# Performance work log

Measured on AMD Instinct MI355X. Metric: run time of the kernel, lower is better.

Reference implementation:

```python
import jax, jax.numpy as jnp
import numpy as np

CH = 128          # channels
R1 = 8            # ch_reduction1 -> theta/phi dim = 16
R2 = 2            # ch_reduction2 -> g dim = 64
D = 2             # downsampling (maxpool kernel/stride on w,h)


def _conv1x1x1(x, w, b):
    # x: (b, cin, n, w, h); w: (cout, cin); b: (cout,)
    return jnp.einsum('bcnwh,oc->bonwh', x, w) + b[None, :, None, None, None]


def _maxpool_wh(x):
    # 2x2 max pool (stride 2) over the last two dims; x: (b, c, n, w, h)
    b, c, n, w, h = x.shape
    return x.reshape(b, c, n, w // D, D, h // D, D).max(axis=(4, 6))


def setup_inputs() -> dict:
    key = jax.random.key(0)
    ks = jax.random.split(key, 9)
    c1, c2 = CH // R1, CH // R2
    s = lambda fan: 1.0 / np.sqrt(fan)
    return {
        'x': jax.random.normal(ks[0], (2, CH, 16, 32, 32), jnp.float32),
        'w_theta': jax.random.normal(ks[1], (c1, CH), jnp.float32) * s(CH),
        'b_theta': jnp.zeros((c1,), jnp.float32),
        'w_phi': jax.random.normal(ks[2], (c1, CH), jnp.float32) * s(CH),
        'b_phi': jnp.zeros((c1,), jnp.float32),
        'w_g': jax.random.normal(ks[3], (c2, CH), jnp.float32) * s(CH),
        'b_g': jnp.zeros((c2,), jnp.float32),
        'w_attn_g': jax.random.normal(ks[4], (CH, c2), jnp.float32) * s(c2),
        'b_attn_g': jnp.zeros((CH,), jnp.float32),
        'gamma': jnp.zeros((1,), jnp.float32),  # initial_gamma = 0
    }


def reference(x, w_theta, b_theta, w_phi, b_phi, w_g, b_g, w_attn_g, b_attn_g, gamma):
    bs, ch, n, w, h = x.shape
    N = n * w * h                       # query locations
    M = n * (w // D) * (h // D)         # pooled key/value locations

    # theta: (bs, N, c1)
    theta = jnp.tanh(_conv1x1x1(x, w_theta, b_theta))
    theta = theta.transpose(0, 2, 3, 4, 1).reshape(bs, N, -1)

    # phi: tanh proj -> maxpool over w,h -> (bs, M, c1)
    phi = _maxpool_wh(jnp.tanh(_conv1x1x1(x, w_phi, b_phi)))
    phi = phi.transpose(0, 2, 3, 4, 1).reshape(bs, M, -1)

    # dot-product kernel; softmax over dim=1 (QUERY axis), as in the torch code
    attn = jax.nn.softmax(jnp.einsum('bnc,bmc->bnm', theta, phi), axis=1)

    # g: proj -> maxpool -> (bs, M, c2)
    g = _maxpool_wh(_conv1x1x1(x, w_g, b_g))
    g = g.transpose(0, 2, 3, 4, 1).reshape(bs, M, -1)

    # attend and fold back to (bs, c2, n, w, h)
    attn_g = jnp.einsum('bnm,bmc->bnc', attn, g)
    attn_g = attn_g.reshape(bs, n, w, h, -1).transpose(0, 4, 1, 2, 3)
    attn_g = _conv1x1x1(attn_g, w_attn_g, b_attn_g)

    alpha = jax.nn.sigmoid(gamma)[0]
    out = (1.0 - alpha) * x + alpha * attn_g
    return (out, attn_g)
```

## Files before the change

### kernel.cpp

```cpp
#include <hip/hip_runtime.h>

typedef short bf16x8 __attribute__((ext_vector_type(8)));
typedef float f32x16 __attribute__((ext_vector_type(16)));

#define DI __device__ __forceinline__

constexpr int BS = 2, CH = 128;
constexpr int NQ = 16384, NM = 4096;
constexpr size_t NX = (size_t)BS * CH * NQ;

DI float bf2f(ushort u) { unsigned v = ((unsigned)u) << 16; return __builtin_bit_cast(float, v); }
DI ushort f2bf(float f) {
  unsigned u = __builtin_bit_cast(unsigned, f);
  u += 0x7FFFu + ((u >> 16) & 1u);
  return (ushort)(u >> 16);
}
DI float ldany(const void* p, size_t i, int f) {
  return f ? ((const float*)p)[i] : bf2f(((const ushort*)p)[i]);
}
DI f32x16 mfma_bf16(bf16x8 a, bf16x8 b, f32x16 c) {
  return __builtin_amdgcn_mfma_f32_32x32x16_bf16(a, b, c, 0, 0, 0);
}
DI float fexp2(float x) { return __builtin_amdgcn_exp2f(x); }

__global__ void k_sniff(const void* __restrict__ x, int* __restrict__ flag) {
  if (threadIdx.x == 0 && blockIdx.x == 0) {
    const ushort* u = (const ushort*)x;
    int garbage = 0, zeros = 0;
    for (int i = 0; i < 256; ++i) {
      float v = bf2f(u[i]);
      if (!(fabsf(v) < 1e9f)) garbage++;
      if ((i & 1) == 0 && u[i] == 0) zeros++;
    }
    flag[0] = (garbage >= 8 || zeros >= 100) ? 1 : 0;
  }
}

__global__ __launch_bounds__(256) void k_prep(
    const void* __restrict__ wT, const void* __restrict__ bT,
    const void* __restrict__ wP, const void* __restrict__ bP,
    const void* __restrict__ wG, const void* __restrict__ bG,
    const void* __restrict__ wAG, const void* __restrict__ bAG,
    const int* __restrict__ flag,
    float* __restrict__ bAllf, uint4* __restrict__ wF, uint4* __restrict__ wBf)
{
  int t = threadIdx.x;
  int f = flag[0];
  if (blockIdx.x == 0) {
    if (t < 16)  bAllf[t]       = ldany(bT, t, f);
    if (t < 16)  bAllf[16 + t]  = ldany(bP, t, f);
    if (t < 64)  bAllf[32 + t]  = ldany(bG, t, f);
    if (t < 128) bAllf[96 + t]  = ldany(bAG, t, f);
  } else if (blockIdx.x <= 4) {
    int idx = (blockIdx.x - 1) * 256 + t;
    int lane = idx & 63, ks = (idx >> 6) & 3, ot = idx >> 8;
    size_t src = (size_t)(ot * 32 + (lane & 31)) * 64 + ks * 16 + (lane >> 5) * 8;
    union { uint4 v4; ushort s[8]; } o;
    #pragma unroll
    for (int j = 0; j < 8; ++j) o.s[j] = f2bf(ldany(wAG, src + j, f));
    wF[idx] = o.v4;
  } else {
    int idx = (int)(blockIdx.x - 5) * 256 + t;
    int kb = idx / 192, rem = idx % 192;
    int ob = rem >> 6, lane = rem & 63;
    int r = ob * 32 + (lane & 31);
    int c = kb * 16 + (lane >> 5) * 8;
    const void* src; int row;
    if (r < 16)      { src = wT; row = r; }
    else if (r < 32) { src = wP; row = r - 16; }
    else             { src = wG; row = r - 32; }
    union { uint4 v4; ushort s[8]; } o;
    #pragma unroll
    for (int j = 0; j < 8; ++j) o.s[j] = f2bf(ldany(src, (size_t)row * 128 + c + j, f));
    wBf[(kb * 3 + ob) * 64 + lane] = o.v4;
  }
}

__global__ __launch_bounds__(128) void k_proj(
    const void* __restrict__ x, const int* __restrict__ flag,
    const uint4* __restrict__ wBf, const float* __restrict__ bAllf,
    ushort* __restrict__ theta, ushort* __restrict__ phi, ushort* __restrict__ gm)
{
  int b = blockIdx.y;
  int qt = blockIdx.x;
  int t = threadIdx.x;
  int w = t >> 6, l = t & 63, lr = l & 31, lh = l >> 5;
  int f = flag[0];

  __shared__ float tile[64][33];

  size_t xbase = (size_t)b * CH * NQ + qt * 64 + w * 32 + lr;

  f32x16 acc0, acc1, acc2;
  #pragma unroll
  for (int i = 0; i < 16; ++i) { acc0[i] = 0.f; acc1[i] = 0.f; acc2[i] = 0.f; }

  #pragma unroll
  for (int kb = 0; kb < 8; ++kb) {
    union { uint4 v4; ushort s[8]; } a;
    int cb = kb * 16 + lh * 8;
    if (f) {
      const float* xf = (const float*)x;
      #pragma unroll
      for (int j = 0; j < 8; ++j) a.s[j] = f2bf(xf[xbase + (size_t)(cb + j) * NQ]);
    } else {
      const ushort* xu = (const ushort*)x;
      #pragma unroll
      for (int j = 0; j < 8; ++j) a.s[j] = xu[xbase + (size_t)(cb + j) * NQ];
    }
    bf16x8 aF = __builtin_bit_cast(bf16x8, a.v4);
    uint4 b0 = wBf[(kb * 3 + 0) * 64 + l];
    uint4 b1 = wBf[(kb * 3 + 1) * 64 + l];
    uint4 b2 = wBf[(kb * 3 + 2) * 64 + l];
    acc0 = mfma_bf16(aF, __builtin_bit_cast(bf16x8, b0), acc0);
    acc1 = mfma_bf16(aF, __builtin_bit_cast(bf16x8, b1), acc1);
    acc2 = mfma_bf16(aF, __builtin_bit_cast(bf16x8, b2), acc2);
  }

  constexpr float L2E = 1.4426950408889634f;

  #pragma unroll
  for (int ob = 0; ob < 3; ++ob) {
    __syncthreads();
    {
      f32x16 A = (ob == 0) ? acc0 : ((ob == 1) ? acc1 : acc2);
      #pragma unroll
      for (int r = 0; r < 16; ++r) {
        int qq = (r & 3) + 8 * (r >> 2) + 4 * lh;
        tile[w * 32 + qq][lr] = A[r];
      }
    }
    __syncthreads();
    if (ob == 0) {
      if (t < 64) {
        union { uint4 v4[2]; ushort s[16]; } th;
        #pragma unroll
        for (int c = 0; c < 16; ++c)
          th.s[c] = f2bf(tanhf(tile[t][c] + bAllf[c]) * L2E);
        uint4* dst = (uint4*)(theta + ((size_t)b * NQ + qt * 64 + t) * 16);
        dst[0] = th.v4[0]; dst[1] = th.v4[1];
      } else {
        int idx = t - 64;
        int m = idx >> 2, c4 = (idx & 3) * 4;
        int h2 = m * 2;
        union { uint2 v2; ushort s[4]; } ph;
        #pragma unroll
        for (int cc = 0; cc < 4; ++cc) {
          int c = 16 + c4 + cc;
          float z = fmaxf(fmaxf(tile[h2][c], tile[h2 + 1][c]),
                          fmaxf(tile[32 + h2][c], tile[32 + h2 + 1][c]));
          ph.s[cc] = f2bf(tanhf(z + bAllf[c]));
        }
        *(uint2*)(phi + ((size_t)b * NM + qt * 16 + m) * 16 + c4) = ph.v2;
      }
    } else {
      int cb = (ob - 1) * 32;
      int m = t >> 3, c4 = (t & 7) * 4;
      int h2 = m * 2;
      union { uint2 v2; ushort s[4]; } gv;
      #pragma unroll
      for (int cc = 0; cc < 4; ++cc) {
        int c = c4 + cc;
        float z = fmaxf(fmaxf(tile[h2][c], tile[h2 + 1][c]),
                        fmaxf(tile[32 + h2][c], tile[32 + h2 + 1][c]));
        gv.s[cc] = f2bf(z + bAllf[32 + cb + c]);
      }
      *(uint2*)(gm + ((size_t)b * NM + qt * 16 + m) * 64 + cb + c4) = gv.v2;
    }
  }
}

__global__ __launch_bounds__(256, 6) void k_denom(
    const ushort* __restrict__ theta, const ushort* __restrict__ phi,
    float* __restrict__ partial)
{
  int b = blockIdx.z, qs = blockIdx.y;
  int w = threadIdx.x >> 6;
  int l = threadIdx.x & 63, lr = l & 31, lh = l >> 5;
  int m0 = blockIdx.x * 128 + w * 32;

  bf16x8 pB = __builtin_bit_cast(bf16x8, *(const uint4*)(phi + ((size_t)b * NM + m0 + lr) * 16 + lh * 8));
  const ushort* thb = theta + ((size_t)b * NQ + qs * 512 + lr) * 16 + lh * 8;

  bf16x8 tA1 = __builtin_bit_cast(bf16x8, *(const uint4*)(thb + 512));
  f32x16 S;
  #pragma unroll
  for (int i = 0; i < 16; ++i) S[i] = 0.f;
  S = mfma_bf16(__builtin_bit_cast(bf16x8, *(const uint4*)thb), pB, S);

  float s = 0.f;
  for (int it = 0; it < 16; ++it) {
    bf16x8 tA2 = __builtin_bit_cast(bf16x8, *(const uint4*)(thb + (size_t)((it + 2) & 15) * 512));
    __builtin_amdgcn_sched_barrier(0);
    f32x16 Sn;
    #pragma unroll
    for (int i = 0; i < 16; ++i) Sn[i] = 0.f;
    Sn = mfma_bf16(tA1, pB, Sn);
    #pragma unroll
    for (int r = 0; r < 16; ++r) s += fexp2(S[r]);
    S = Sn; tA1 = tA2;
  }
  s += __shfl_xor(s, 32, 64);
  if (l < 32) partial[(((size_t)b * 32 + qs) << 12) + m0 + lr] = s;
}

__global__ __launch_bounds__(256) void k_gsf(
    const float* __restrict__ partial, const ushort* __restrict__ gm,
    uint4* __restrict__ gsF)
{
  int b = blockIdx.y, mb = blockIdx.x;
  int t = threadIdx.x;
  int mbase = mb * 32;

  __shared__ float dinv_sh[32];
  __shared__ float tile[32][65];

  if (t < 32) {
    int m = mbase + t;
    float s = 0.f;
    #pragma unroll
    for (int p = 0; p < 32; ++p) s += partial[(((size_t)b * 32 + p) << 12) + m];
    dinv_sh[t] = 1.f / s;
  }
  __syncthreads();

  {
    int m_loc = t >> 3, c = (t & 7) * 8;
    union { uint4 v4; ushort s[8]; } v;
    v.v4 = *(const uint4*)(gm + ((size_t)b * NM + mbase + m_loc) * 64 + c);
    float dv = dinv_sh[m_loc];
    #pragma unroll
    for (int j = 0; j < 8; ++j) tile[m_loc][c + j] = bf2f(v.s[j]) * dv;
  }
  __syncthreads();

  int ms_loc = t >> 7, ct = (t >> 6) & 1, lane = t & 63;
  int col = ct * 32 + (lane & 31);
  int rbase = ms_loc * 16 + (lane >> 5) * 8;
  union { uint4 v4; ushort s[8]; } o;
  #pragma unroll
  for (int j = 0; j < 8; ++j) o.s[j] = f2bf(tile[rbase + j][col]);
  int ms = (mbase >> 4) + ms_loc;
  gsF[(((size_t)b * 256 + ms) * 2 + ct) * 64 + lane] = o.v4;
}

__global__ __launch_bounds__(256, 4) void k_attn(
    const ushort* __restrict__ theta, const ushort* __restrict__ phi,
    const uint4* __restrict__ gsF, const uint4* __restrict__ wF,
    const float* __restrict__ bAllf, const void* __restrict__ x,
    const void* __restrict__ gamma, const int* __restrict__ flag,
    void* __restrict__ out_base)
{
  int b = blockIdx.y;
  int q0 = blockIdx.x * 32;
  int t = threadIdx.x;
  int mq = t >> 6, l = t & 63, lr = l & 31, lh = l >> 5;

  __shared__ float agPart[4][32][65];
  __shared__ __align__(16) ushort agF[32][80];

  bf16x8 tB = __builtin_bit_cast(bf16x8, *(const uint4*)(theta + ((size_t)b * NQ + q0 + lr) * 16 + lh * 8));

  const ushort* phb = phi + ((size_t)b * NM + lr) * 16 + lh * 8;
  const uint4* gF = gsF + (size_t)b * 32768;

  f32x16 acc0, acc1;
  #pragma unroll
  for (int i = 0; i < 16; ++i) { acc0[i] = 0.f; acc1[i] = 0.f; }

  size_t gb0 = (size_t)(mq * 2) * 128;
  uint4 g00 = gF[gb0 + l];
  uint4 g01 = gF[gb0 + 64 + l];
  uint4 g10 = gF[gb0 + 128 + l];
  uint4 g11 = gF[gb0 + 192 + l];
  bf16x8 pAn = __builtin_bit_cast(bf16x8, *(const uint4*)(phb + (size_t)(mq * 32 + 128) * 16));
  f32x16 S;
  #pragma unroll
  for (int i = 0; i < 16; ++i) S[i] = 0.f;
  S = mfma_bf16(__builtin_bit_cast(bf16x8, *(const uint4*)(phb + (size_t)(mq * 32) * 16)), tB, S);

  for (int it = 0; it < 32; ++it) {
    int it1 = (it + 1) & 31, it2 = (it + 2) & 31;
    size_t gb = (size_t)(mq * 2 + it1 * 8) * 128;
    uint4 n00 = gF[gb + l];
    uint4 n01 = gF[gb + 64 + l];
    uint4 n10 = gF[gb + 128 + l];
    uint4 n11 = gF[gb + 192 + l];
    bf16x8 pA2 = __builtin_bit_cast(bf16x8, *(const uint4*)(phb + (size_t)(mq * 32 + it2 * 128) * 16));
    __builtin_amdgcn_sched_barrier(0);

    f32x16 Sn;
    #pragma unroll
    for (int i = 0; i < 16; ++i) Sn[i] = 0.f;
    Sn = mfma_bf16(pAn, tB, Sn);
    __builtin_amdgcn_sched_barrier(0);

    #pragma unroll
    for (int r = 0; r < 16; ++r) S[r] = fexp2(S[r]);

    uint u0, u1, u2, u3, u4, u5, u6, u7;
    asm("v_cvt_pk_bf16_f32 %0, %1, %2" : "=v"(u0) : "v"(S[0]),  "v"(S[1]));
    asm("v_cvt_pk_bf16_f32 %0, %1, %2" : "=v"(u1) : "v"(S[2]),  "v"(S[3]));
    asm("v_cvt_pk_bf16_f32 %0, %1, %2" : "=v"(u2) : "v"(S[4]),  "v"(S[5]));
    asm("v_cvt_pk_bf16_f32 %0, %1, %2" : "=v"(u3) : "v"(S[6]),  "v"(S[7]));
    asm("v_cvt_pk_bf16_f32 %0, %1, %2" : "=v"(u4) : "v"(S[8]),  "v"(S[9]));
    asm("v_cvt_pk_bf16_f32 %0, %1, %2" : "=v"(u5) : "v"(S[10]), "v"(S[11]));
    asm("v_cvt_pk_bf16_f32 %0, %1, %2" : "=v"(u6) : "v"(S[12]), "v"(S[13]));
    asm("v_cvt_pk_bf16_f32 %0, %1, %2" : "=v"(u7) : "v"(S[14]), "v"(S[15]));

    asm("v_permlane32_swap_b32 %0, %1" : "+v"(u0), "+v"(u2));
    asm("v_permlane32_swap_b32 %0, %1" : "+v"(u1), "+v"(u3));
    asm("v_permlane32_swap_b32 %0, %1" : "+v"(u4), "+v"(u6));
    asm("v_permlane32_swap_b32 %0, %1" : "+v"(u5), "+v"(u7));

    uint4 fa0 = make_uint4(u0, u1, u2, u3);
    uint4 fa1 = make_uint4(u4, u5, u6, u7);

    acc0 = mfma_bf16(__builtin_bit_cast(bf16x8, fa0), __builtin_bit_cast(bf16x8, g00), acc0);
    acc1 = mfma_bf16(__builtin_bit_cast(bf16x8, fa0), __builtin_bit_cast(bf16x8, g01), acc1);
    acc0 = mfma_bf16(__builtin_bit_cast(bf16x8, fa1), __builtin_bit_cast(bf16x8, g10), acc0);
    acc1 = mfma_bf16(__builtin_bit_cast(bf16x8, fa1), __builtin_bit_cast(bf16x8, g11), acc1);

    S = Sn; pAn = pA2;
    g00 = n00; g01 = n01; g10 = n10; g11 = n11;
  }

  int mode = flag[0];
  float ga = ldany(gamma, 0, mode);
  float alpha = 1.f / (1.f + __expf(-ga));

  #pragma unroll
  for (int r = 0; r < 16; ++r) {
    int qq = (r & 3) + 8 * (r >> 2) + 4 * lh;
    agPart[mq][qq][lr]      = acc0[r];
    agPart[mq][qq][32 + lr] = acc1[r];
  }
  __syncthreads();
  {
    #pragma unroll
    for (int jj = 0; jj < 8; ++jj) {
      int c = mq * 16 + lh * 8 + jj;
      float vsum = agPart[0][lr][c] + agPart[1][lr][c] + agPart[2][lr][c] + agPart[3][lr][c];
      agF[lr][c] = f2bf(vsum);
    }
  }
  __syncthreads();
  {
    f32x16 oacc;
    #pragma unroll
    for (int i = 0; i < 16; ++i) oacc[i] = 0.f;
    #pragma unroll
    for (int ks = 0; ks < 4; ++ks) {
      bf16x8 aw = __builtin_bit_cast(bf16x8, wF[(mq * 4 + ks) * 64 + l]);
      bf16x8 bg = __builtin_bit_cast(bf16x8, *(const uint4*)&agF[lr][ks * 16 + lh * 8]);
      oacc = mfma_bf16(aw, bg, oacc);
    }
    if (mode) {
      float* o0 = (float*)out_base;
      float* o1 = o0 + NX;
      const float* xf = (const float*)x;
      #pragma unroll
      for (int r = 0; r < 16; ++r) {
        int o = mq * 32 + (r & 3) + 8 * (r >> 2) + 4 * lh;
        size_t oi = ((size_t)b * CH + o) * NQ + q0 + lr;
        float ag = oacc[r] + bAllf[96 + o];
        o0[oi] = (1.f - alpha) * xf[oi] + alpha * ag;
        o1[oi] = ag;
      }
    } else {
      ushort* o0 = (ushort*)out_base;
      ushort* o1 = o0 + NX;
      const ushort* xu = (const ushort*)x;
      #pragma unroll
      for (int r = 0; r < 16; ++r) {
        int o = mq * 32 + (r & 3) + 8 * (r >> 2) + 4 * lh;
        size_t oi = ((size_t)b * CH + o) * NQ + q0 + lr;
        float ag = oacc[r] + bAllf[96 + o];
        o0[oi] = f2bf((1.f - alpha) * bf2f(xu[oi]) + alpha * ag);
        o1[oi] = f2bf(ag);
      }
    }
  }
}

extern "C" void kernel_launch(void* const* d_in, const int* in_sizes, int n_in,
                              void* d_out, int out_size, void* d_ws, size_t ws_size,
                              hipStream_t stream) {
  const void* x    = d_in[0];
  const void* wT   = d_in[1];
  const void* bT   = d_in[2];
  const void* wP   = d_in[3];
  const void* bP   = d_in[4];
  const void* wG   = d_in[5];
  const void* bG   = d_in[6];
  const void* wAG  = d_in[7];
  const void* bAG  = d_in[8];
  const void* gmm  = d_in[9];

  char* ws = (char*)d_ws;
  ushort* theta  = (ushort*)(ws + 0);
  ushort* phi    = (ushort*)(ws + 1048576);
  ushort* gm     = (ushort*)(ws + 1310720);
  float*  part   = (float*) (ws + 2359296);
  uint4*  gsF    = (uint4*) (ws + 3407872);
  uint4*  wF     = (uint4*) (ws + 4456448);
  uint4*  wBf    = (uint4*) (ws + 4472832);
  float*  bAllf  = (float*) (ws + 4497408);
  int*    flag   = (int*)   (ws + 4498432);

  k_sniff<<<dim3(1), dim3(64), 0, stream>>>(x, flag);
  k_prep<<<dim3(11), dim3(256), 0, stream>>>(wT, bT, wP, bP, wG, bG, wAG, bAG, flag, bAllf, wF, wBf);
  k_proj<<<dim3(256, 2), dim3(128), 0, stream>>>(x, flag, wBf, bAllf, theta, phi, gm);
  k_denom<<<dim3(32, 32, 2), dim3(256), 0, stream>>>(theta, phi, part);
  k_gsf<<<dim3(128, 2), dim3(256), 0, stream>>>(part, gm, gsF);
  k_attn<<<dim3(512, 2), dim3(256), 0, stream>>>(theta, phi, gsF, wF, bAllf, x, gmm, flag, d_out);
}
```

Measured before the change: 82.70 us.

## Process 64 queries per attention block to reuse g and phi fragments

Each k_attn block now handles two 32-query tiles, reusing each loaded phi fragment and g fragment for two score MFMAs and two sets of accumulators. This halves the global loads of g and phi per query and halves the grid. The software-pipelined score computation (S computed one iteration ahead) is dropped in favour of computing two independent score tiles per iteration. Occupancy is lowered to 3 blocks per CU to fit the extra accumulators, and the epilogue loops over the two halves.

```diff
diff --git a/kernel.cpp b/kernel.cpp
--- a/kernel.cpp
+++ b/kernel.cpp
@@ -244,7 +244,7 @@
   gsF[(((size_t)b * 256 + ms) * 2 + ct) * 64 + lane] = o.v4;
 }
 
-__global__ __launch_bounds__(256, 4) void k_attn(
+__global__ __launch_bounds__(256, 3) void k_attn(
     const ushort* __restrict__ theta, const ushort* __restrict__ phi,
     const uint4* __restrict__ gsF, const uint4* __restrict__ wF,
     const float* __restrict__ bAllf, const void* __restrict__ x,
@@ -252,76 +252,95 @@
     void* __restrict__ out_base)
 {
   int b = blockIdx.y;
-  int q0 = blockIdx.x * 32;
+  int q0 = blockIdx.x * 64;
   int t = threadIdx.x;
   int mq = t >> 6, l = t & 63, lr = l & 31, lh = l >> 5;
 
   __shared__ float agPart[4][32][65];
   __shared__ __align__(16) ushort agF[32][80];
 
-  bf16x8 tB = __builtin_bit_cast(bf16x8, *(const uint4*)(theta + ((size_t)b * NQ + q0 + lr) * 16 + lh * 8));
+  bf16x8 tB0 = __builtin_bit_cast(bf16x8, *(const uint4*)(theta + ((size_t)b * NQ + q0 + lr) * 16 + lh * 8));
+  bf16x8 tB1 = __builtin_bit_cast(bf16x8, *(const uint4*)(theta + ((size_t)b * NQ + q0 + 32 + lr) * 16 + lh * 8));
 
   const ushort* phb = phi + ((size_t)b * NM + lr) * 16 + lh * 8;
   const uint4* gF = gsF + (size_t)b * 32768;
 
-  f32x16 acc0, acc1;
-  #pragma unroll
-  for (int i = 0; i < 16; ++i) { acc0[i] = 0.f; acc1[i] = 0.f; }
+  f32x16 a00, a01, a10, a11;
+  #pragma unroll
+  for (int i = 0; i < 16; ++i) { a00[i] = 0.f; a01[i] = 0.f; a10[i] = 0.f; a11[i] = 0.f; }
+  f32x16 zero16;
+  #pragma unroll
+  for (int i = 0; i < 16; ++i) zero16[i] = 0.f;
 
   size_t gb0 = (size_t)(mq * 2) * 128;
   uint4 g00 = gF[gb0 + l];
   uint4 g01 = gF[gb0 + 64 + l];
   uint4 g10 = gF[gb0 + 128 + l];
   uint4 g11 = gF[gb0 + 192 + l];
-  bf16x8 pAn = __builtin_bit_cast(bf16x8, *(const uint4*)(phb + (size_t)(mq * 32 + 128) * 16));
-  f32x16 S;
-  #pragma unroll
-  for (int i = 0; i < 16; ++i) S[i] = 0.f;
-  S = mfma_bf16(__builtin_bit_cast(bf16x8, *(const uint4*)(phb + (size_t)(mq * 32) * 16)), tB, S);
+  bf16x8 pA = __builtin_bit_cast(bf16x8, *(const uint4*)(phb + (size_t)(mq * 32) * 16));
 
   for (int it = 0; it < 32; ++it) {
-    int it1 = (it + 1) & 31, it2 = (it + 2) & 31;
+    int it1 = (it + 1) & 31;
     size_t gb = (size_t)(mq * 2 + it1 * 8) * 128;
     uint4 n00 = gF[gb + l];
     uint4 n01 = gF[gb + 64 + l];
     uint4 n10 = gF[gb + 128 + l];
     uint4 n11 = gF[gb + 192 + l];
-    bf16x8 pA2 = __builtin_bit_cast(bf16x8, *(const uint4*)(phb + (size_t)(mq * 32 + it2 * 128) * 16));
+    bf16x8 pAn = __builtin_bit_cast(bf16x8, *(const uint4*)(phb + (size_t)(mq * 32 + it1 * 128) * 16));
     __builtin_amdgcn_sched_barrier(0);
 
-    f32x16 Sn;
-    #pragma unroll
-    for (int i = 0; i < 16; ++i) Sn[i] = 0.f;
-    Sn = mfma_bf16(pAn, tB, Sn);
-    __builtin_amdgcn_sched_barrier(0);
-
-    #pragma unroll
-    for (int r = 0; r < 16; ++r) S[r] = fexp2(S[r]);
+    f32x16 Sa = mfma_bf16(pA, tB0, zero16);
+    f32x16 Sb = mfma_bf16(pA, tB1, zero16);
 
     uint u0, u1, u2, u3, u4, u5, u6, u7;
-    asm("v_cvt_pk_bf16_f32 %0, %1, %2" : "=v"(u0) : "v"(S[0]),  "v"(S[1]));
-    asm("v_cvt_pk_bf16_f32 %0, %1, %2" : "=v"(u1) : "v"(S[2]),  "v"(S[3]));
-    asm("v_cvt_pk_bf16_f32 %0, %1, %2" : "=v"(u2) : "v"(S[4]),  "v"(S[5]));
-    asm("v_cvt_pk_bf16_f32 %0, %1, %2" : "=v"(u3) : "v"(S[6]),  "v"(S[7]));
-    asm("v_cvt_pk_bf16_f32 %0, %1, %2" : "=v"(u4) : "v"(S[8]),  "v"(S[9]));
-    asm("v_cvt_pk_bf16_f32 %0, %1, %2" : "=v"(u5) : "v"(S[10]), "v"(S[11]));
-    asm("v_cvt_pk_bf16_f32 %0, %1, %2" : "=v"(u6) : "v"(S[12]), "v"(S[13]));
-    asm("v_cvt_pk_bf16_f32 %0, %1, %2" : "=v"(u7) : "v"(S[14]), "v"(S[15]));
-
+
+    #pragma unroll
+    for (int r = 0; r < 16; ++r) Sa[r] = fexp2(Sa[r]);
+    asm("v_cvt_pk_bf16_f32 %0, %1, %2" : "=v"(u0) : "v"(Sa[0]),  "v"(Sa[1]));
+    asm("v_cvt_pk_bf16_f32 %0, %1, %2" : "=v"(u1) : "v"(Sa[2]),  "v"(Sa[3]));
+    asm("v_cvt_pk_bf16_f32 %0, %1, %2" : "=v"(u2) : "v"(Sa[4]),  "v"(Sa[5]));
+    asm("v_cvt_pk_bf16_f32 %0, %1, %2" : "=v"(u3) : "v"(Sa[6]),  "v"(Sa[7]));
+    asm("v_cvt_pk_bf16_f32 %0, %1, %2" : "=v"(u4) : "v"(Sa[8]),  "v"(Sa[9]));
+    asm("v_cvt_pk_bf16_f32 %0, %1, %2" : "=v"(u5) : "v"(Sa[10]), "v"(Sa[11]));
+    asm("v_cvt_pk_bf16_f32 %0, %1, %2" : "=v"(u6) : "v"(Sa[12]), "v"(Sa[13]));
+    asm("v_cvt_pk_bf16_f32 %0, %1, %2" : "=v"(u7) : "v"(Sa[14]), "v"(Sa[15]));
     asm("v_permlane32_swap_b32 %0, %1" : "+v"(u0), "+v"(u2));
     asm("v_permlane32_swap_b32 %0, %1" : "+v"(u1), "+v"(u3));
     asm("v_permlane32_swap_b32 %0, %1" : "+v"(u4), "+v"(u6));
     asm("v_permlane32_swap_b32 %0, %1" : "+v"(u5), "+v"(u7));
-
-    uint4 fa0 = make_uint4(u0, u1, u2, u3);
-    uint4 fa1 = make_uint4(u4, u5, u6, u7);
-
-    acc0 = mfma_bf16(__builtin_bit_cast(bf16x8, fa0), __builtin_bit_cast(bf16x8, g00), acc0);
-    acc1 = mfma_bf16(__builtin_bit_cast(bf16x8, fa0), __builtin_bit_cast(bf16x8, g01), acc1);
-    acc0 = mfma_bf16(__builtin_bit_cast(bf16x8, fa1), __builtin_bit_cast(bf16x8, g10), acc0);
-    acc1 = mfma_bf16(__builtin_bit_cast(bf16x8, fa1), __builtin_bit_cast(bf16x8, g11), acc1);
-
-    S = Sn; pAn = pA2;
+    {
+      uint4 fa0 = make_uint4(u0, u1, u2, u3);
+      uint4 fa1 = make_uint4(u4, u5, u6, u7);
+      a00 = mfma_bf16(__builtin_bit_cast(bf16x8, fa0), __builtin_bit_cast(bf16x8, g00), a00);
+      a01 = mfma_bf16(__builtin_bit_cast(bf16x8, fa0), __builtin_bit_cast(bf16x8, g01), a01);
+      a00 = mfma_bf16(__builtin_bit_cast(bf16x8, fa1), __builtin_bit_cast(bf16x8, g10), a00);
+      a01 = mfma_bf16(__builtin_bit_cast(bf16x8, fa1), __builtin_bit_cast(bf16x8, g11), a01);
+    }
+
+    #pragma unroll
+    for (int r = 0; r < 16; ++r) Sb[r] = fexp2(Sb[r]);
+    asm("v_cvt_pk_bf16_f32 %0, %1, %2" : "=v"(u0) : "v"(Sb[0]),  "v"(Sb[1]));
+    asm("v_cvt_pk_bf16_f32 %0, %1, %2" : "=v"(u1) : "v"(Sb[2]),  "v"(Sb[3]));
+    asm("v_cvt_pk_bf16_f32 %0, %1, %2" : "=v"(u2) : "v"(Sb[4]),  "v"(Sb[5]));
+    asm("v_cvt_pk_bf16_f32 %0, %1, %2" : "=v"(u3) : "v"(Sb[6]),  "v"(Sb[7]));
+    asm("v_cvt_pk_bf16_f32 %0, %1, %2" : "=v"(u4) : "v"(Sb[8]),  "v"(Sb[9]));
+    asm("v_cvt_pk_bf16_f32 %0, %1, %2" : "=v"(u5) : "v"(Sb[10]), "v"(Sb[11]));
+    asm("v_cvt_pk_bf16_f32 %0, %1, %2" : "=v"(u6) : "v"(Sb[12]), "v"(Sb[13]));
+    asm("v_cvt_pk_bf16_f32 %0, %1, %2" : "=v"(u7) : "v"(Sb[14]), "v"(Sb[15]));
+    asm("v_permlane32_swap_b32 %0, %1" : "+v"(u0), "+v"(u2));
+    asm("v_permlane32_swap_b32 %0, %1" : "+v"(u1), "+v"(u3));
+    asm("v_permlane32_swap_b32 %0, %1" : "+v"(u4), "+v"(u6));
+    asm("v_permlane32_swap_b32 %0, %1" : "+v"(u5), "+v"(u7));
+    {
+      uint4 fb0 = make_uint4(u0, u1, u2, u3);
+      uint4 fb1 = make_uint4(u4, u5, u6, u7);
+      a10 = mfma_bf16(__builtin_bit_cast(bf16x8, fb0), __builtin_bit_cast(bf16x8, g00), a10);
+      a11 = mfma_bf16(__builtin_bit_cast(bf16x8, fb0), __builtin_bit_cast(bf16x8, g01), a11);
+      a10 = mfma_bf16(__builtin_bit_cast(bf16x8, fb1), __builtin_bit_cast(bf16x8, g10), a10);
+      a11 = mfma_bf16(__builtin_bit_cast(bf16x8, fb1), __builtin_bit_cast(bf16x8, g11), a11);
+    }
+
+    pA = pAn;
     g00 = n00; g01 = n01; g10 = n10; g11 = n11;
   }
 
@@ -330,54 +349,62 @@
   float alpha = 1.f / (1.f + __expf(-ga));
 
   #pragma unroll
-  for (int r = 0; r < 16; ++r) {
-    int qq = (r & 3) + 8 * (r >> 2) + 4 * lh;
-    agPart[mq][qq][lr]      = acc0[r];
-    agPart[mq][qq][32 + lr] = acc1[r];
-  }
-  __syncthreads();
-  {
-    #pragma unroll
-    for (int jj = 0; jj < 8; ++jj) {
-      int c = mq * 16 + lh * 8 + jj;
-      float vsum = agPart[0][lr][c] + agPart[1][lr][c] + agPart[2][lr][c] + agPart[3][lr][c];
-      agF[lr][c] = f2bf(vsum);
-    }
-  }
-  __syncthreads();
-  {
-    f32x16 oacc;
-    #pragma unroll
-    for (int i = 0; i < 16; ++i) oacc[i] = 0.f;
-    #pragma unroll
-    for (int ks = 0; ks < 4; ++ks) {
-      bf16x8 aw = __builtin_bit_cast(bf16x8, wF[(mq * 4 + ks) * 64 + l]);
-      bf16x8 bg = __builtin_bit_cast(bf16x8, *(const uint4*)&agF[lr][ks * 16 + lh * 8]);
-      oacc = mfma_bf16(aw, bg, oacc);
-    }
-    if (mode) {
-      float* o0 = (float*)out_base;
-      float* o1 = o0 + NX;
-      const float* xf = (const float*)x;
+  for (int h = 0; h < 2; ++h) {
+    __syncthreads();
+    {
+      f32x16 ac0 = (h == 0) ? a00 : a10;
+      f32x16 ac1 = (h == 0) ? a01 : a11;
       #pragma unroll
       for (int r = 0; r < 16; ++r) {
-        int o = mq * 32 + (r & 3) + 8 * (r >> 2) + 4 * lh;
-        size_t oi = ((size_t)b * CH + o) * NQ + q0 + lr;
-        float ag = oacc[r] + bAllf[96 + o];
-        o0[oi] = (1.f - alpha) * xf[oi] + alpha * ag;
-        o1[oi] = ag;
-      }
-    } else {
-      ushort* o0 = (ushort*)out_base;
-      ushort* o1 = o0 + NX;
-      const ushort* xu = (const ushort*)x;
-      #pragma unroll
-      for (int r = 0; r < 16; ++r) {
-        int o = mq * 32 + (r & 3) + 8 * (r >> 2) + 4 * lh;
-        size_t oi = ((size_t)b * CH + o) * NQ + q0 + lr;
-        float ag = oacc[r] + bAllf[96 + o];
-        o0[oi] = f2bf((1.f - alpha) * bf2f(xu[oi]) + alpha * ag);
-        o1[oi] = f2bf(ag);
+        int qq = (r & 3) + 8 * (r >> 2) + 4 * lh;
+        agPart[mq][qq][lr]      = ac0[r];
+        agPart[mq][qq][32 + lr] = ac1[r];
+      }
+    }
+    __syncthreads();
+    {
+      #pragma unroll
+      for (int jj = 0; jj < 8; ++jj) {
+        int c = mq * 16 + lh * 8 + jj;
+        float vsum = agPart[0][lr][c] + agPart[1][lr][c] + agPart[2][lr][c] + agPart[3][lr][c];
+        agF[lr][c] = f2bf(vsum);
+      }
+    }
+    __syncthreads();
+    {
+      f32x16 oacc;
+      #pragma unroll
+      for (int i = 0; i < 16; ++i) oacc[i] = 0.f;
+      #pragma unroll
+      for (int ks = 0; ks < 4; ++ks) {
+        bf16x8 aw = __builtin_bit_cast(bf16x8, wF[(mq * 4 + ks) * 64 + l]);
+        bf16x8 bg = __builtin_bit_cast(bf16x8, *(const uint4*)&agF[lr][ks * 16 + lh * 8]);
+        oacc = mfma_bf16(aw, bg, oacc);
+      }
+      if (mode) {
+        float* o0 = (float*)out_base;
+        float* o1 = o0 + NX;
+        const float* xf = (const float*)x;
+        #pragma unroll
+        for (int r = 0; r < 16; ++r) {
+          int o = mq * 32 + (r & 3) + 8 * (r >> 2) + 4 * lh;
+          size_t oi = ((size_t)b * CH + o) * NQ + q0 + h * 32 + lr;
+          float ag = oacc[r] + bAllf[96 + o];
+          o0[oi] = (1.f - alpha) * xf[oi] + alpha * ag;
+          o1[oi] = ag;
+        }
+      } else {
+        ushort* o0 = (ushort*)out_base;
+        ushort* o1 = o0 + NX;
+        const ushort* xu = (const ushort*)x;
+        #pragma unroll
+        for (int r = 0; r < 16; ++r) {
+          int o = mq * 32 + (r & 3) + 8 * (r >> 2) + 4 * lh;
+          size_t oi = ((size_t)b * CH + o) * NQ + q0 + h * 32 + lr;
+          float ag = oacc[r] + bAllf[96 + o];
+          o0[oi] = f2bf((1.f - alpha) * bf2f(xu[oi]) + alpha * ag);
+          o1[oi] = f2bf(ag);
+        }
       }
     }
   }
@@ -413,5 +440,5 @@
   k_proj<<<dim3(256, 2), dim3(128), 0, stream>>>(x, flag, wBf, bAllf, theta, phi, gm);
   k_denom<<<dim3(32, 32, 2), dim3(256), 0, stream>>>(theta, phi, part);
   k_gsf<<<dim3(128, 2), dim3(256), 0, stream>>>(part, gm, gsF);
-  k_attn<<<dim3(512, 2), dim3(256), 0, stream>>>(theta, phi, gsF, wF, bAllf, x, gmm, flag, d_out);
-}
+  k_attn<<<dim3(256, 2), dim3(256), 0, stream>>>(theta, phi, gsF, wF, bAllf, x, gmm, flag, d_out);
+}
```

Measured after the change: 78.97 us. 1.05x faster.
